# Kernel tuning notes

Measured on AMD Instinct MI355X. Metric: run time of the kernel, lower is better.

Reference implementation:

```python
import jax, jax.numpy as jnp
import numpy as np

N_NODES = 50000
N_EDGES = 800000
IN_CH = 64
OUT_CH = 64
NHEAD = 8


def _edge_softmax(e, dst, num_nodes):
    # segment softmax over incoming edges of each destination node,
    # elementwise over [H, D] feature dims (matches dgl edge_softmax)
    mx = jax.ops.segment_max(e, dst, num_segments=num_nodes)
    mx = jax.lax.stop_gradient(mx)
    ex = jnp.exp(e - mx[dst])
    s = jax.ops.segment_sum(ex, dst, num_segments=num_nodes)
    return ex / s[dst]


def setup_inputs() -> dict:
    key = jax.random.key(0)
    ks = jax.random.split(key, 10)
    ndata = jax.random.normal(ks[0], (N_NODES, IN_CH), dtype=jnp.float32)
    src = jax.random.randint(ks[1], (N_EDGES,), 0, N_NODES)
    dst = jax.random.randint(ks[2], (N_EDGES,), 0, N_NODES)
    sc = 1.0 / np.sqrt(IN_CH)
    W1 = jax.random.normal(ks[3], (IN_CH, OUT_CH), dtype=jnp.float32) * sc
    b1 = jnp.zeros((OUT_CH,), dtype=jnp.float32)
    W2 = jax.random.normal(ks[4], (IN_CH, OUT_CH), dtype=jnp.float32) * sc
    b2 = jnp.zeros((OUT_CH,), dtype=jnp.float32)
    Wres = jax.random.normal(ks[5], (IN_CH, OUT_CH), dtype=jnp.float32) * sc
    bres = jnp.zeros((OUT_CH,), dtype=jnp.float32)
    m = jnp.ones((3, NHEAD, OUT_CH // NHEAD), dtype=jnp.float32)
    return {"ndata": ndata, "src": src, "dst": dst, "W1": W1, "b1": b1,
            "W2": W2, "b2": b2, "Wres": Wres, "bres": bres, "m": m}


def reference(ndata, src, dst, W1, b1, W2, b2, Wres, bres, m):
    N = ndata.shape[0]
    H = NHEAD
    # add self loops (dgl.add_self_loop)
    loop = jnp.arange(N, dtype=src.dtype)
    s = jnp.concatenate([src, loop])
    d = jnp.concatenate([dst, loop])
    # minmax_norm over last dim
    mn = jnp.min(ndata, axis=-1, keepdims=True)
    mx = jnp.max(ndata, axis=-1, keepdims=True)
    x = (ndata - mn) / (mx - mn + 1e-5)
    # node projections -> [N, H, Dh]
    l = (x @ W1 + b1).reshape(N, H, -1)
    r = (x @ W2 + b2).reshape(N, H, -1)
    # edge-wise fused activation of src+dst (acfun='sigmoid')
    le = jax.nn.sigmoid(l[s] + l[d])
    re = jax.nn.sigmoid(r[s] + r[d])
    # edge softmax grouped by destination
    le = _edge_softmax(le, d, N)
    re = _edge_softmax(re, d, N)
    # two-hop scatter-gather aggregation
    ft_r = jax.ops.segment_sum(r[s] * le, d, num_segments=N)   # [N,H,Dh]
    ft_l = jax.ops.segment_sum(ft_r[s] * re, d, num_segments=N)
    h = (m[0] * ft_l).reshape(N, -1) + (x @ Wres + bres)
    return h
```

## Files before the change

### kernel.cpp

```cpp
#include <hip/hip_runtime.h>
#include <hip/hip_fp16.h>

#define CH 64
#define LOG2E  1.44269504f
#define MLOG2E -1.44269504f

__device__ __forceinline__ float exp2fast(float x) {
    float r; asm("v_exp_f32 %0, %1" : "=v"(r) : "v"(x)); return r;
}

__global__ void count_kernel(const int* __restrict__ dst, int* __restrict__ deg,
                             int* __restrict__ rank, int E)
{
    for (int i = blockIdx.x * blockDim.x + threadIdx.x; i < E;
         i += gridDim.x * blockDim.x) {
        rank[i] = atomicAdd(&deg[dst[i]], 1);
    }
}

__global__ __launch_bounds__(256) void proj_kernel(
    const float* __restrict__ nd,
    const float* __restrict__ W1, const float* __restrict__ b1,
    const float* __restrict__ W2, const float* __restrict__ b2,
    const float* __restrict__ Wr, const float* __restrict__ br,
    __half2* __restrict__ lr, float* __restrict__ hres, int N)
{
    __shared__ __align__(16) float xs[4][CH];
    const int lane = threadIdx.x & 63;
    const int wid  = threadIdx.x >> 6;

    float w1[CH], w2[CH], wr[CH];
#pragma unroll
    for (int i = 0; i < CH; ++i) {
        w1[i] = W1[i * CH + lane];
        w2[i] = W2[i * CH + lane];
        wr[i] = Wr[i * CH + lane];
    }
    const float bb1 = b1[lane], bb2 = b2[lane], bbr = br[lane];

    const int nwave = gridDim.x * 4;
    for (int node = blockIdx.x * 4 + wid; node < N; node += nwave) {
        const unsigned row = (unsigned)node * CH;
        float v = nd[row + lane];
        float mn = v, mx = v;
#pragma unroll
        for (int off = 32; off; off >>= 1) {
            mn = fminf(mn, __shfl_xor(mn, off));
            mx = fmaxf(mx, __shfl_xor(mx, off));
        }
        float x = (v - mn) / (mx - mn + 1e-5f);
        xs[wid][lane] = x;
        float a1 = bb1, a2 = bb2, a3 = bbr;
        const float4* x4 = reinterpret_cast<const float4*>(&xs[wid][0]);
#pragma unroll
        for (int k = 0; k < CH / 4; ++k) {
            float4 xv = x4[k];
            a1 = fmaf(xv.x, w1[4*k+0], a1);
            a1 = fmaf(xv.y, w1[4*k+1], a1);
            a1 = fmaf(xv.z, w1[4*k+2], a1);
            a1 = fmaf(xv.w, w1[4*k+3], a1);
            a2 = fmaf(xv.x, w2[4*k+0], a2);
            a2 = fmaf(xv.y, w2[4*k+1], a2);
            a2 = fmaf(xv.z, w2[4*k+2], a2);
            a2 = fmaf(xv.w, w2[4*k+3], a2);
            a3 = fmaf(xv.x, wr[4*k+0], a3);
            a3 = fmaf(xv.y, wr[4*k+1], a3);
            a3 = fmaf(xv.z, wr[4*k+2], a3);
            a3 = fmaf(xv.w, wr[4*k+3], a3);
        }
        lr[row + lane]   = __floats2half2_rn(a1, a2);
        hres[row + lane] = a3;
    }
}

__global__ __launch_bounds__(256) void bsum_kernel(
    const int* __restrict__ deg, int* __restrict__ bsum, int N)
{
    __shared__ int ws[4];
    int i = blockIdx.x * 256 + threadIdx.x;
    int lane = threadIdx.x & 63, wid = threadIdx.x >> 6;
    int v = (i < N) ? deg[i] : 0;
#pragma unroll
    for (int off = 32; off; off >>= 1) v += __shfl_xor(v, off);
    if (lane == 0) ws[wid] = v;
    __syncthreads();
    if (threadIdx.x == 0) bsum[blockIdx.x] = ws[0] + ws[1] + ws[2] + ws[3];
}

__global__ __launch_bounds__(64) void bscan_kernel(int* __restrict__ bsum, int nb)
{
    int lane = threadIdx.x;
    int carry = 0;
    for (int base = 0; base < nb; base += 64) {
        int i = base + lane;
        int v = (i < nb) ? bsum[i] : 0;
        int s = v;
#pragma unroll
        for (int off = 1; off < 64; off <<= 1) {
            int t = __shfl_up(s, off);
            if (lane >= off) s += t;
        }
        if (i < nb) bsum[i] = carry + s - v;
        carry += __shfl(s, 63);
    }
}

__global__ __launch_bounds__(256) void apply_kernel(
    const int* __restrict__ deg, const int* __restrict__ bsum,
    int* __restrict__ rowptr, int N, int total)
{
    __shared__ int ws[4];
    int i = blockIdx.x * 256 + threadIdx.x;
    int lane = threadIdx.x & 63, wid = threadIdx.x >> 6;
    int v = (i < N) ? deg[i] : 0;
    int s = v;
#pragma unroll
    for (int off = 1; off < 64; off <<= 1) {
        int t = __shfl_up(s, off);
        if (lane >= off) s += t;
    }
    if (lane == 63) ws[wid] = s;
    __syncthreads();
    int woff = 0;
    for (int w = 0; w < wid; ++w) woff += ws[w];
    int excl = bsum[blockIdx.x] + woff + s - v;
    if (i < N) rowptr[i] = excl;
    if (blockIdx.x == 0 && threadIdx.x == 0) rowptr[N] = total;
}

__global__ void scatter_kernel(const int* __restrict__ src,
                               const int* __restrict__ dst,
                               const int* __restrict__ rank,
                               const int* __restrict__ rowptr,
                               int* __restrict__ col, int E)
{
    for (int i = blockIdx.x * blockDim.x + threadIdx.x; i < E;
         i += gridDim.x * blockDim.x) {
        col[rowptr[dst[i]] + rank[i]] = src[i];
    }
}

#define EDGE_BATCH(U_, TBL_, STEP_)                                          \
    {                                                                        \
        __half2 hb[U_];                                                      \
        _Pragma("unroll")                                                    \
        for (int u = 0; u < (U_); ++u) {                                     \
            int s_ = __builtin_amdgcn_readlane(myc, j + u);                  \
            hb[u] = TBL_[(unsigned)(s_ * CH) + lane];                        \
        }                                                                    \
        _Pragma("unroll")                                                    \
        for (int u = 0; u < (U_); ++u) { STEP_(hb[u]); }                     \
        j += (U_);                                                           \
    }

__global__ __launch_bounds__(256) void passA_kernel(
    const __half2* __restrict__ lr,
    const int* __restrict__ rowptr, const int* __restrict__ col,
    __half2* __restrict__ rf, int N)
{
    const int node = blockIdx.x * 4 + (threadIdx.x >> 6);
    const int lane = threadIdx.x & 63;
    if (node >= N) return;
    const unsigned row = (unsigned)node * CH;
    const float2 own = __half22float2(lr[row + lane]);
    const float l_d = own.x, r_d = own.y;
    const float nl_d = MLOG2E * l_d;
    const int beg = rowptr[node], end = rowptr[node + 1];

    float wl = exp2fast(LOG2E * __builtin_amdgcn_rcpf(1.f + exp2fast(2.f * nl_d)));
    float denL = wl, acc = r_d * wl;

#define A_STEP(H_) {                                                         \
        float2 f = __half22float2(H_);                                       \
        float uu = exp2fast(fmaf(f.x, MLOG2E, nl_d));                        \
        float w  = exp2fast(LOG2E * __builtin_amdgcn_rcpf(1.f + uu));        \
        denL += w; acc = fmaf(f.y, w, acc); }

    int e = beg;
    while (e < end) {
        int cnt = end - e; if (cnt > 64) cnt = 64;
        int idx = e + lane; if (idx >= end) idx = end - 1;
        const int myc = col[idx];
        int j = 0;
        int nfull = cnt >> 4;
        for (int b = 0; b < nfull; ++b) EDGE_BATCH(16, lr, A_STEP)
        if (cnt & 8) EDGE_BATCH(8, lr, A_STEP)
        if (cnt & 4) EDGE_BATCH(4, lr, A_STEP)
        if (cnt & 2) EDGE_BATCH(2, lr, A_STEP)
        if (cnt & 1) EDGE_BATCH(1, lr, A_STEP)
        e += cnt;
    }
    rf[row + lane] = __floats2half2_rn(r_d, acc / denL);
}

__global__ __launch_bounds__(256) void passB_kernel(
    const __half2* __restrict__ rf,
    const int* __restrict__ rowptr, const int* __restrict__ col,
    const float* __restrict__ m0, float* __restrict__ out, int N)
{
    const int node = blockIdx.x * 4 + (threadIdx.x >> 6);
    const int lane = threadIdx.x & 63;
    if (node >= N) return;
    const unsigned row = (unsigned)node * CH;
    const float2 own = __half22float2(rf[row + lane]);
    const float r_d = own.x, f_own = own.y;
    const float nr_d = MLOG2E * r_d;
    const int beg = rowptr[node], end = rowptr[node + 1];

    float wsl = exp2fast(LOG2E * __builtin_amdgcn_rcpf(1.f + exp2fast(2.f * nr_d)));
    float dR = wsl, acc = f_own * wsl;

#define B_STEP(H_) {                                                         \
        float2 f = __half22float2(H_);                                       \
        float uu = exp2fast(fmaf(f.x, MLOG2E, nr_d));                        \
        float w  = exp2fast(LOG2E * __builtin_amdgcn_rcpf(1.f + uu));        \
        dR += w; acc = fmaf(f.y, w, acc); }

    int e = beg;
    while (e < end) {
        int cnt = end - e; if (cnt > 64) cnt = 64;
        int idx = e + lane; if (idx >= end) idx = end - 1;
        const int myc = col[idx];
        int j = 0;
        int nfull = cnt >> 4;
        for (int b = 0; b < nfull; ++b) EDGE_BATCH(16, rf, B_STEP)
        if (cnt & 8) EDGE_BATCH(8, rf, B_STEP)
        if (cnt & 4) EDGE_BATCH(4, rf, B_STEP)
        if (cnt & 2) EDGE_BATCH(2, rf, B_STEP)
        if (cnt & 1) EDGE_BATCH(1, rf, B_STEP)
        e += cnt;
    }
    out[row + lane] = fmaf(m0[lane], acc / dR, out[row + lane]);
}

extern "C" void kernel_launch(void* const* d_in, const int* in_sizes, int n_in,
                              void* d_out, int out_size, void* d_ws, size_t ws_size,
                              hipStream_t stream)
{
    const float* ndata = (const float*)d_in[0];
    const int*   src   = (const int*)d_in[1];
    const int*   dst   = (const int*)d_in[2];
    const float* W1    = (const float*)d_in[3];
    const float* b1    = (const float*)d_in[4];
    const float* W2    = (const float*)d_in[5];
    const float* b2    = (const float*)d_in[6];
    const float* Wr    = (const float*)d_in[7];
    const float* br    = (const float*)d_in[8];
    const float* m     = (const float*)d_in[9];
    float* out = (float*)d_out;

    const int N = in_sizes[0] / CH;
    const int E = in_sizes[1];
    const int nbk = (N + 255) / 256;

    char* ws = (char*)d_ws;
    size_t off = 0;
    auto alloc = [&](size_t bytes) -> void* {
        void* p = ws + off;
        off = (off + bytes + 255) & ~(size_t)255;
        return p;
    };
    __half2* lr   = (__half2*)alloc((size_t)N * CH * 4);
    __half2* rf   = (__half2*)alloc((size_t)N * CH * 4);
    int*   deg    = (int*)alloc((size_t)N * 4);
    int*   bsum   = (int*)alloc((size_t)nbk * 4);
    int*   rowptr = (int*)alloc((size_t)(N + 1) * 4);
    int*   rank   = (int*)alloc((size_t)E * 4);
    int*   col    = (int*)alloc((size_t)E * 4);

    hipMemsetAsync(deg, 0, (size_t)N * 4, stream);
    count_kernel<<<2048, 256, 0, stream>>>(dst, deg, rank, E);
    proj_kernel<<<1024, 256, 0, stream>>>(ndata, W1, b1, W2, b2, Wr, br,
                                          lr, out, N);
    bsum_kernel<<<nbk, 256, 0, stream>>>(deg, bsum, N);
    bscan_kernel<<<1, 64, 0, stream>>>(bsum, nbk);
    apply_kernel<<<nbk, 256, 0, stream>>>(deg, bsum, rowptr, N, E);
    scatter_kernel<<<2048, 256, 0, stream>>>(src, dst, rank, rowptr, col, E);
    int nb = (N + 3) / 4;
    passA_kernel<<<nb, 256, 0, stream>>>(lr, rowptr, col, rf, N);
    passB_kernel<<<nb, 256, 0, stream>>>(rf, rowptr, col, m, out, N);
}
```

Baseline: 236.5 us.

## Fuse degree count into projection, use single-pass lookback scan, polynomial exp

Merges the degree-counting atomics into the projection launch by giving them extra blocks, so the two independent workloads share one grid. The three-kernel prefix sum becomes a single-pass decoupled-lookback scan that uses ticket-ordered blocks and flags zeroed by the same memset. The sigmoid-then-exp edge weight now uses a cubic polynomial for exp on [0,1] in place of a second v_exp. This cuts kernel launches and transcendental work, at the cost of a spin-wait in the scan and a small approximation error in the softmax weights.

```diff
diff --git a/kernel.cpp b/kernel.cpp
--- a/kernel.cpp
+++ b/kernel.cpp
@@ -4,27 +4,38 @@
 #define CH 64
 #define LOG2E  1.44269504f
 #define MLOG2E -1.44269504f
+#define PROJ_BLOCKS 1024
 
 __device__ __forceinline__ float exp2fast(float x) {
     float r; asm("v_exp_f32 %0, %1" : "=v"(r) : "v"(x)); return r;
 }
 
-__global__ void count_kernel(const int* __restrict__ dst, int* __restrict__ deg,
-                             int* __restrict__ rank, int E)
-{
-    for (int i = blockIdx.x * blockDim.x + threadIdx.x; i < E;
-         i += gridDim.x * blockDim.x) {
-        rank[i] = atomicAdd(&deg[dst[i]], 1);
-    }
-}
-
-__global__ __launch_bounds__(256) void proj_kernel(
+#define EXPP_D0 0.9994851f
+#define EXPP_D1 1.0160896f
+#define EXPP_D2 0.4230492f
+#define EXPP_D3 0.2790848f
+__device__ __forceinline__ float exp01_poly(float s) {
+    return fmaf(fmaf(fmaf(EXPP_D3, s, EXPP_D2), s, EXPP_D1), s, EXPP_D0);
+}
+
+__global__ __launch_bounds__(256) void proj_count_kernel(
     const float* __restrict__ nd,
     const float* __restrict__ W1, const float* __restrict__ b1,
     const float* __restrict__ W2, const float* __restrict__ b2,
     const float* __restrict__ Wr, const float* __restrict__ br,
-    __half2* __restrict__ lr, float* __restrict__ hres, int N)
-{
+    __half2* __restrict__ lr, float* __restrict__ hres,
+    const int* __restrict__ dst, int* __restrict__ deg,
+    int* __restrict__ rank, int N, int E)
+{
+    if (blockIdx.x >= PROJ_BLOCKS) {
+        const int stride = (gridDim.x - PROJ_BLOCKS) * 256;
+        for (int i = (blockIdx.x - PROJ_BLOCKS) * 256 + threadIdx.x; i < E;
+             i += stride) {
+            rank[i] = atomicAdd(&deg[dst[i]], 1);
+        }
+        return;
+    }
+
     __shared__ __align__(16) float xs[4][CH];
     const int lane = threadIdx.x & 63;
     const int wid  = threadIdx.x >> 6;
@@ -38,7 +49,7 @@
     }
     const float bb1 = b1[lane], bb2 = b2[lane], bbr = br[lane];
 
-    const int nwave = gridDim.x * 4;
+    const int nwave = PROJ_BLOCKS * 4;
     for (int node = blockIdx.x * 4 + wid; node < N; node += nwave) {
         const unsigned row = (unsigned)node * CH;
         float v = nd[row + lane];
@@ -73,45 +84,19 @@
     }
 }
 
-__global__ __launch_bounds__(256) void bsum_kernel(
-    const int* __restrict__ deg, int* __restrict__ bsum, int N)
-{
+__global__ __launch_bounds__(256) void scan_kernel(
+    const int* __restrict__ deg, int* __restrict__ rowptr,
+    int* __restrict__ agg, int* __restrict__ pre, int* __restrict__ flag,
+    int* __restrict__ ticket, int N, int total)
+{
+    __shared__ int chunk;
     __shared__ int ws[4];
-    int i = blockIdx.x * 256 + threadIdx.x;
-    int lane = threadIdx.x & 63, wid = threadIdx.x >> 6;
-    int v = (i < N) ? deg[i] : 0;
-#pragma unroll
-    for (int off = 32; off; off >>= 1) v += __shfl_xor(v, off);
-    if (lane == 0) ws[wid] = v;
+    __shared__ int prefix_sh;
+    if (threadIdx.x == 0) chunk = atomicAdd(ticket, 1);
     __syncthreads();
-    if (threadIdx.x == 0) bsum[blockIdx.x] = ws[0] + ws[1] + ws[2] + ws[3];
-}
-
-__global__ __launch_bounds__(64) void bscan_kernel(int* __restrict__ bsum, int nb)
-{
-    int lane = threadIdx.x;
-    int carry = 0;
-    for (int base = 0; base < nb; base += 64) {
-        int i = base + lane;
-        int v = (i < nb) ? bsum[i] : 0;
-        int s = v;
-#pragma unroll
-        for (int off = 1; off < 64; off <<= 1) {
-            int t = __shfl_up(s, off);
-            if (lane >= off) s += t;
-        }
-        if (i < nb) bsum[i] = carry + s - v;
-        carry += __shfl(s, 63);
-    }
-}
-
-__global__ __launch_bounds__(256) void apply_kernel(
-    const int* __restrict__ deg, const int* __restrict__ bsum,
-    int* __restrict__ rowptr, int N, int total)
-{
-    __shared__ int ws[4];
-    int i = blockIdx.x * 256 + threadIdx.x;
-    int lane = threadIdx.x & 63, wid = threadIdx.x >> 6;
+    const int b = chunk;
+    const int i = b * 256 + threadIdx.x;
+    const int lane = threadIdx.x & 63, wid = threadIdx.x >> 6;
     int v = (i < N) ? deg[i] : 0;
     int s = v;
 #pragma unroll
@@ -123,9 +108,34 @@
     __syncthreads();
     int woff = 0;
     for (int w = 0; w < wid; ++w) woff += ws[w];
-    int excl = bsum[blockIdx.x] + woff + s - v;
+    const int blocksum = ws[0] + ws[1] + ws[2] + ws[3];
+
+    if (threadIdx.x == 0) {
+        __hip_atomic_store(&agg[b], blocksum, __ATOMIC_RELEASE, __HIP_MEMORY_SCOPE_AGENT);
+        __hip_atomic_store(&flag[b], 1, __ATOMIC_RELEASE, __HIP_MEMORY_SCOPE_AGENT);
+        int running = 0;
+        if (b > 0) {
+            int j = b - 1;
+            while (true) {
+                int f = __hip_atomic_load(&flag[j], __ATOMIC_ACQUIRE, __HIP_MEMORY_SCOPE_AGENT);
+                if (f == 2) {
+                    running += __hip_atomic_load(&pre[j], __ATOMIC_ACQUIRE, __HIP_MEMORY_SCOPE_AGENT);
+                    break;
+                } else if (f == 1) {
+                    running += __hip_atomic_load(&agg[j], __ATOMIC_ACQUIRE, __HIP_MEMORY_SCOPE_AGENT);
+                    if (j == 0) break;
+                    --j;
+                }
+            }
+        }
+        __hip_atomic_store(&pre[b], running + blocksum, __ATOMIC_RELEASE, __HIP_MEMORY_SCOPE_AGENT);
+        __hip_atomic_store(&flag[b], 2, __ATOMIC_RELEASE, __HIP_MEMORY_SCOPE_AGENT);
+        prefix_sh = running;
+    }
+    __syncthreads();
+    const int excl = prefix_sh + woff + s - v;
     if (i < N) rowptr[i] = excl;
-    if (blockIdx.x == 0 && threadIdx.x == 0) rowptr[N] = total;
+    if (b == 0 && threadIdx.x == 0) rowptr[N] = total;
 }
 
 __global__ void scatter_kernel(const int* __restrict__ src,
@@ -167,13 +177,13 @@
     const float nl_d = MLOG2E * l_d;
     const int beg = rowptr[node], end = rowptr[node + 1];
 
-    float wl = exp2fast(LOG2E * __builtin_amdgcn_rcpf(1.f + exp2fast(2.f * nl_d)));
+    float wl = exp01_poly(__builtin_amdgcn_rcpf(1.f + exp2fast(2.f * nl_d)));
     float denL = wl, acc = r_d * wl;
 
 #define A_STEP(H_) {                                                         \
         float2 f = __half22float2(H_);                                       \
-        float uu = exp2fast(fmaf(f.x, MLOG2E, nl_d));                        \
-        float w  = exp2fast(LOG2E * __builtin_amdgcn_rcpf(1.f + uu));        \
+        float sg = __builtin_amdgcn_rcpf(1.f + exp2fast(fmaf(f.x, MLOG2E, nl_d))); \
+        float w  = exp01_poly(sg);                                           \
         denL += w; acc = fmaf(f.y, w, acc); }
 
     int e = beg;
@@ -207,13 +217,13 @@
     const float nr_d = MLOG2E * r_d;
     const int beg = rowptr[node], end = rowptr[node + 1];
 
-    float wsl = exp2fast(LOG2E * __builtin_amdgcn_rcpf(1.f + exp2fast(2.f * nr_d)));
+    float wsl = exp01_poly(__builtin_amdgcn_rcpf(1.f + exp2fast(2.f * nr_d)));
     float dR = wsl, acc = f_own * wsl;
 
 #define B_STEP(H_) {                                                         \
         float2 f = __half22float2(H_);                                       \
-        float uu = exp2fast(fmaf(f.x, MLOG2E, nr_d));                        \
-        float w  = exp2fast(LOG2E * __builtin_amdgcn_rcpf(1.f + uu));        \
+        float sg = __builtin_amdgcn_rcpf(1.f + exp2fast(fmaf(f.x, MLOG2E, nr_d))); \
+        float w  = exp01_poly(sg);                                           \
         dR += w; acc = fmaf(f.y, w, acc); }
 
     int e = beg;
@@ -262,19 +272,21 @@
     };
     __half2* lr   = (__half2*)alloc((size_t)N * CH * 4);
     __half2* rf   = (__half2*)alloc((size_t)N * CH * 4);
-    int*   deg    = (int*)alloc((size_t)N * 4);
-    int*   bsum   = (int*)alloc((size_t)nbk * 4);
+    int*   deg    = (int*)alloc((size_t)(N + nbk + 1) * 4);
+    int*   flag   = deg + N;
+    int*   ticket = deg + N + nbk;
+    size_t zbytes = (size_t)(N + nbk + 1) * 4;
+    int*   agg    = (int*)alloc((size_t)nbk * 4);
+    int*   pre    = (int*)alloc((size_t)nbk * 4);
     int*   rowptr = (int*)alloc((size_t)(N + 1) * 4);
     int*   rank   = (int*)alloc((size_t)E * 4);
     int*   col    = (int*)alloc((size_t)E * 4);
 
-    hipMemsetAsync(deg, 0, (size_t)N * 4, stream);
-    count_kernel<<<2048, 256, 0, stream>>>(dst, deg, rank, E);
-    proj_kernel<<<1024, 256, 0, stream>>>(ndata, W1, b1, W2, b2, Wr, br,
-                                          lr, out, N);
-    bsum_kernel<<<nbk, 256, 0, stream>>>(deg, bsum, N);
-    bscan_kernel<<<1, 64, 0, stream>>>(bsum, nbk);
-    apply_kernel<<<nbk, 256, 0, stream>>>(deg, bsum, rowptr, N, E);
+    hipMemsetAsync(deg, 0, zbytes, stream);
+    proj_count_kernel<<<PROJ_BLOCKS + 2048, 256, 0, stream>>>(
+        ndata, W1, b1, W2, b2, Wr, br, lr, out, dst, deg, rank, N, E);
+    scan_kernel<<<nbk, 256, 0, stream>>>(deg, rowptr, agg, pre, flag, ticket,
+                                         N, E);
     scatter_kernel<<<2048, 256, 0, stream>>>(src, dst, rank, rowptr, col, E);
     int nb = (N + 3) / 4;
     passA_kernel<<<nb, 256, 0, stream>>>(lr, rowptr, col, rf, N);
```

After: 300.6 us. +27.1%, slower.
